# Kernel tuning notes

Hardware: AMD Instinct MI355X
Metric: run time of the kernel (lower is better)

The kernel has to match this reference:

```python
import jax, jax.numpy as jnp
import numpy as np

B, S, D = 2, 1024, 1024
H, KV, HD = 16, 4, 64
E, F = 8, 3584
EPS = 1e-5
TOP_K = 2


def setup_inputs() -> dict:
    key = jax.random.key(0)
    ks = jax.random.split(key, 12)
    sc = 0.02
    inv_freq = 1.0 / (10000.0 ** (np.arange(0, HD, 2, dtype=np.float32) / HD))
    freqs = np.outer(np.arange(S, dtype=np.float32), inv_freq)
    emb = np.concatenate([freqs, freqs], axis=-1)  # [S, HD]
    return {
        'x': jax.random.normal(ks[0], (B, S, D), jnp.float32),
        'ln1_w': jnp.ones((D,), jnp.float32),
        'ln2_w': jnp.ones((D,), jnp.float32),
        'wq': jax.random.normal(ks[1], (H * HD, D), jnp.float32) * sc,
        'wk': jax.random.normal(ks[2], (KV * HD, D), jnp.float32) * sc,
        'wv': jax.random.normal(ks[3], (KV * HD, D), jnp.float32) * sc,
        'wo': jax.random.normal(ks[4], (D, H * HD), jnp.float32) * sc,
        'gate_w': jax.random.normal(ks[5], (E, D), jnp.float32) * sc,
        'w1': jax.random.normal(ks[6], (E, F, D), jnp.float32) * sc,
        'w2': jax.random.normal(ks[7], (E, D, F), jnp.float32) * sc,
        'w3': jax.random.normal(ks[8], (E, F, D), jnp.float32) * sc,
        'cos': jnp.asarray(np.cos(emb)),
        'sin': jnp.asarray(np.sin(emb)),
    }


def _rms_norm(x, w):
    var = jnp.mean(jnp.square(x), axis=-1, keepdims=True)
    return x * jax.lax.rsqrt(var + EPS) * w


def _rotate_half(x):
    x1, x2 = jnp.split(x, 2, axis=-1)
    return jnp.concatenate([-x2, x1], axis=-1)


def _attn(h, wq, wk, wv, wo, cos, sin):
    # h: [B,S,D]
    q = (h @ wq.T).reshape(B, S, H, HD).transpose(0, 2, 1, 3)      # [B,H,S,HD]
    k = (h @ wk.T).reshape(B, S, KV, HD).transpose(0, 2, 1, 3)     # [B,KV,S,HD]
    v = (h @ wv.T).reshape(B, S, KV, HD).transpose(0, 2, 1, 3)
    c = cos[None, None, :S, :]
    s = sin[None, None, :S, :]
    q = q * c + _rotate_half(q) * s
    k = k * c + _rotate_half(k) * s
    k = jnp.repeat(k, H // KV, axis=1)  # GQA expand -> [B,H,S,HD]
    v = jnp.repeat(v, H // KV, axis=1)
    scores = jnp.einsum('bhqd,bhkd->bhqk', q, k) / jnp.sqrt(jnp.float32(HD))
    causal = jnp.tril(jnp.ones((S, S), bool))
    scores = jnp.where(causal[None, None], scores, jnp.float32(-1e30))
    probs = jax.nn.softmax(scores, axis=-1)
    out = jnp.einsum('bhqk,bhkd->bhqd', probs, v)
    out = out.transpose(0, 2, 1, 3).reshape(B, S, H * HD)
    return out @ wo.T


def _moe(h, gate_w, w1, w2, w3):
    T = B * S
    hs = h.reshape(T, D)
    probs = jax.nn.softmax(hs @ gate_w.T, axis=-1)       # [T,E]
    _, sel = jax.lax.top_k(probs, TOP_K)                  # [T,2]
    rw = jnp.take_along_axis(probs, sel, axis=-1)
    rw = rw / jnp.sum(rw, axis=-1, keepdims=True)
    cw = jnp.zeros((T, E), hs.dtype).at[jnp.arange(T)[:, None], sel].add(rw)  # [T,E] combine weights
    h1 = jnp.einsum('td,efd->tef', hs, w1)               # [T,E,F]
    h3 = jnp.einsum('td,efd->tef', hs, w3)
    inter = jax.nn.silu(h1) * h3
    out = jnp.einsum('tef,edf,te->td', inter, w2, cw)
    return out.reshape(B, S, D)


def reference(x, ln1_w, ln2_w, wq, wk, wv, wo, gate_w, w1, w2, w3, cos, sin):
    h = x + _attn(_rms_norm(x, ln1_w), wq, wk, wv, wo, cos, sin)
    h = h + _moe(_rms_norm(h, ln2_w), gate_w, w1, w2, w3)
    return h
```

## Files before the change

kernel.cpp:

```cpp
#include <hip/hip_runtime.h>

typedef unsigned short u16;
using short8 = __attribute__((ext_vector_type(8))) short;
using f32x4  = __attribute__((ext_vector_type(4))) float;

#define TQ   2048
#define DM   1024
#define SLEN 1024
#define FDIM 3584
#define NEXP 8

static __device__ __forceinline__ u16 f2bf(float f) {
  union { float f; unsigned u; } a; a.f = f;
  unsigned r = a.u + 0x7fffu + ((a.u >> 16) & 1u);
  return (u16)(r >> 16);
}
static __device__ __forceinline__ float bf2f(u16 u) {
  union { unsigned u; float f; } a; a.u = ((unsigned)u) << 16;
  return a.f;
}
static __device__ __forceinline__ unsigned cvtpk(float lo, float hi) {
  unsigned r;
  asm volatile("v_cvt_pk_bf16_f32 %0, %1, %2" : "=v"(r) : "v"(lo), "v"(hi));
  return r;
}

static __device__ __forceinline__ void gload16(const void* g, void* l) {
  __builtin_amdgcn_global_load_lds((const __attribute__((address_space(1))) void*)g,
                                   (__attribute__((address_space(3))) void*)l, 16, 0, 0);
}

static __device__ __forceinline__ int swz64(int bid) {
  return (bid & ~63) | ((bid & 7) << 3) | ((bid >> 3) & 7);
}

static __device__ __forceinline__ void cvtwr8(float4 a, float4 b, u16* dst) {
  uint4 u;
  u.x = cvtpk(a.x, a.y); u.y = cvtpk(a.z, a.w);
  u.z = cvtpk(b.x, b.y); u.w = cvtpk(b.z, b.w);
  *(uint4*)dst = u;
}

__global__ __launch_bounds__(256) void rmsnorm_kernel(
    const float* __restrict__ x, const float* __restrict__ w,
    u16* __restrict__ oh, u16* __restrict__ ol, float* __restrict__ of) {
  int t = blockIdx.x, tid = threadIdx.x;
  const float4* xr = (const float4*)(x + (size_t)t * DM);
  float4 v = xr[tid];
  float ss = v.x * v.x + v.y * v.y + v.z * v.z + v.w * v.w;
#pragma unroll
  for (int m = 1; m < 64; m <<= 1) ss += __shfl_xor(ss, m);
  __shared__ float red[4];
  if ((tid & 63) == 0) red[tid >> 6] = ss;
  __syncthreads();
  float tot = red[0] + red[1] + red[2] + red[3];
  float sc = rsqrtf(tot * (1.0f / DM) + 1e-5f);
  float4 wv = ((const float4*)w)[tid];
  float o0 = v.x * sc * wv.x, o1 = v.y * sc * wv.y, o2 = v.z * sc * wv.z, o3 = v.w * sc * wv.w;
  ushort4 hh;
  hh.x = f2bf(o0); hh.y = f2bf(o1); hh.z = f2bf(o2); hh.w = f2bf(o3);
  *(ushort4*)(oh + (size_t)t * DM + tid * 4) = hh;
  if (ol) {
    ushort4 ll;
    ll.x = f2bf(o0 - bf2f(hh.x)); ll.y = f2bf(o1 - bf2f(hh.y));
    ll.z = f2bf(o2 - bf2f(hh.z)); ll.w = f2bf(o3 - bf2f(hh.w));
    *(ushort4*)(ol + (size_t)t * DM + tid * 4) = ll;
  }
  if (of) {
    float4 o4; o4.x = o0; o4.y = o1; o4.z = o2; o4.w = o3;
    ((float4*)(of + (size_t)t * DM))[tid] = o4;
  }
}

__global__ __launch_bounds__(256) void wconv_split_kernel(
    const float* __restrict__ wq, const float* __restrict__ wk,
    const float* __restrict__ wv, const float* __restrict__ wo,
    u16* __restrict__ qkvh, u16* __restrict__ qkvl,
    u16* __restrict__ woh, u16* __restrict__ wol) {
  for (int i = blockIdx.x * 256 + threadIdx.x; i < 655360; i += 640 * 256) {
    int el = i * 4;
    const float* src; u16 *dh, *dl;
    if (el < 1572864) {
      int r = el >> 10, c = el & 1023;
      if (r < 1024) src = wq + el;
      else if (r < 1280) src = wk + (r - 1024) * 1024 + c;
      else src = wv + (r - 1280) * 1024 + c;
      dh = qkvh + el; dl = qkvl + el;
    } else {
      int e2 = el - 1572864;
      src = wo + e2; dh = woh + e2; dl = wol + e2;
    }
    float4 v = *(const float4*)src;
    ushort4 h, l;
    h.x = f2bf(v.x); h.y = f2bf(v.y); h.z = f2bf(v.z); h.w = f2bf(v.w);
    l.x = f2bf(v.x - bf2f(h.x)); l.y = f2bf(v.y - bf2f(h.y));
    l.z = f2bf(v.z - bf2f(h.z)); l.w = f2bf(v.w - bf2f(h.w));
    *(ushort4*)dh = h; *(ushort4*)dl = l;
  }
}

template <bool RESID>
__global__ __launch_bounds__(256) void gemm_split2_kernel(
    const u16* __restrict__ Ah, const u16* __restrict__ Al,
    const u16* __restrict__ Wh, const u16* __restrict__ Wl,
    float* __restrict__ C, const float* __restrict__ resid, int N) {
  __shared__ u16 sAh[2][128][32], sAl[2][128][32], sWh[2][64][32], sWl[2][64][32];
  int lid = swz64(blockIdx.x);
  int bm = lid & 15, bn = lid >> 4;
  int tid = threadIdx.x, lane = tid & 63, w = tid >> 6;
  int wm = w >> 1, wn = w & 1;
  int qi = lane & 15, g = lane >> 4;
  int lr = lane >> 2, lc = (lane & 3) * 8;
  const u16* pa0 = Ah + (size_t)(bm * 128 + w * 16 + lr) * DM + lc;
  const u16* pa1 = pa0 + 64 * DM;
  const u16* pl0 = Al + (size_t)(bm * 128 + w * 16 + lr) * DM + lc;
  const u16* pl1 = pl0 + 64 * DM;
  const u16* pw  = Wh + (size_t)(bn * 64 + w * 16 + lr) * DM + lc;
  const u16* pwl = Wl + (size_t)(bn * 64 + w * 16 + lr) * DM + lc;
  f32x4 acc[4][2] = {};
#define STG2(buf, kk) do { \
    gload16(pa0 + (kk), &sAh[buf][w * 16][0]); \
    gload16(pa1 + (kk), &sAh[buf][64 + w * 16][0]); \
    gload16(pl0 + (kk), &sAl[buf][w * 16][0]); \
    gload16(pl1 + (kk), &sAl[buf][64 + w * 16][0]); \
    gload16(pw  + (kk), &sWh[buf][w * 16][0]); \
    gload16(pwl + (kk), &sWl[buf][w * 16][0]); } while (0)
  STG2(0, 0);
  asm volatile("s_waitcnt vmcnt(0)" ::: "memory");
  __syncthreads();
  for (int ks = 0; ks < 32; ks++) {
    int cur = ks & 1;
    if (ks < 31) STG2(cur ^ 1, (ks + 1) * 32);
    short8 afh[4], afl[4], bfh[2], bfl[2];
#pragma unroll
    for (int i = 0; i < 4; i++) {
      afh[i] = *(short8*)&sAh[cur][wm * 64 + i * 16 + qi][g * 8];
      afl[i] = *(short8*)&sAl[cur][wm * 64 + i * 16 + qi][g * 8];
    }
#pragma unroll
    for (int i = 0; i < 2; i++) {
      bfh[i] = *(short8*)&sWh[cur][wn * 32 + i * 16 + qi][g * 8];
      bfl[i] = *(short8*)&sWl[cur][wn * 32 + i * 16 + qi][g * 8];
    }
#pragma unroll
    for (int mi = 0; mi < 4; mi++)
#pragma unroll
      for (int ni = 0; ni < 2; ni++) {
        f32x4 a = acc[mi][ni];
        a = __builtin_amdgcn_mfma_f32_16x16x32_bf16(afh[mi], bfh[ni], a, 0, 0, 0);
        a = __builtin_amdgcn_mfma_f32_16x16x32_bf16(afl[mi], bfh[ni], a, 0, 0, 0);
        a = __builtin_amdgcn_mfma_f32_16x16x32_bf16(afh[mi], bfl[ni], a, 0, 0, 0);
        acc[mi][ni] = a;
      }
    asm volatile("s_waitcnt vmcnt(0)" ::: "memory");
    __syncthreads();
  }
#undef STG2
#pragma unroll
  for (int mi = 0; mi < 4; mi++)
#pragma unroll
    for (int ni = 0; ni < 2; ni++) {
      int col = bn * 64 + wn * 32 + ni * 16 + qi;
#pragma unroll
      for (int r = 0; r < 4; r++) {
        int row = bm * 128 + wm * 64 + mi * 16 + g * 4 + r;
        float val = acc[mi][ni][r];
        if (RESID) val += resid[(size_t)row * N + col];
        C[(size_t)row * N + col] = val;
      }
    }
}

__global__ __launch_bounds__(256) void rope_split_kernel(
    const float* __restrict__ qkvf,
    const float* __restrict__ cosT, const float* __restrict__ sinT,
    u16* __restrict__ qh, u16* __restrict__ ql, u16* __restrict__ kh, u16* __restrict__ kl,
    u16* __restrict__ vh, u16* __restrict__ vl) {
  int t = blockIdx.x, tid = threadIdx.x;
  int s = t & (SLEN - 1);
  const float* rowp = qkvf + (size_t)t * 1536;
#pragma unroll
  for (int it = 0; it < 2; it++) {
    int i = it * 256 + tid;
    int hh = i >> 5, d = i & 31;
    float c = cosT[s * 64 + d], sn = sinT[s * 64 + d];
    size_t dst = (size_t)t * DM + hh * 64 + d;
    float x1 = rowp[hh * 64 + d], x2 = rowp[hh * 64 + d + 32];
    float o1 = x1 * c - x2 * sn;
    float o2 = x2 * c + x1 * sn;
    u16 h1 = f2bf(o1), h2 = f2bf(o2);
    qh[dst] = h1; qh[dst + 32] = h2;
    ql[dst] = f2bf(o1 - bf2f(h1)); ql[dst + 32] = f2bf(o2 - bf2f(h2));
  }
  if (tid < 128) {
    int hh = tid >> 5, d = tid & 31;
    float c = cosT[s * 64 + d], sn = sinT[s * 64 + d];
    size_t dst = (size_t)t * 256 + hh * 64 + d;
    float x1 = rowp[1024 + hh * 64 + d], x2 = rowp[1024 + hh * 64 + d + 32];
    float o1 = x1 * c - x2 * sn;
    float o2 = x2 * c + x1 * sn;
    u16 h1 = f2bf(o1), h2 = f2bf(o2);
    kh[dst] = h1; kh[dst + 32] = h2;
    kl[dst] = f2bf(o1 - bf2f(h1)); kl[dst + 32] = f2bf(o2 - bf2f(h2));
  }
  {
    size_t dst = (size_t)t * 256 + tid;
    float v = rowp[1280 + tid];
    u16 h = f2bf(v);
    vh[dst] = h; vl[dst] = f2bf(v - bf2f(h));
  }
}

__global__ __launch_bounds__(256) void attn_kernel(
    const u16* __restrict__ qh, const u16* __restrict__ ql,
    const u16* __restrict__ kh, const u16* __restrict__ kl,
    const u16* __restrict__ vh, const u16* __restrict__ vl,
    u16* __restrict__ oh, u16* __restrict__ ol) {
  __shared__ u16 sKh[64][72], sKl[64][72];
  __shared__ u16 sVh[64][72], sVl[64][72];
  __shared__ u16 sPh[4][16][72], sPl[4][16][72];
  int qt = blockIdx.x & 15;
  int bh = blockIdx.x >> 4;
  int b = bh >> 4, h = bh & 15, kvh = h >> 2;
  int tid = threadIdx.x, lane = tid & 63, w = tid >> 6;
  int qi = lane & 15, g = lane >> 4;
  int qrow = qt * 64 + w * 16 + qi;
  size_t qbase = ((size_t)(b * SLEN + qrow)) * DM + h * 64;
  short8 qfh[2], qfl[2];
#pragma unroll
  for (int ds = 0; ds < 2; ds++) {
    qfh[ds] = *(const short8*)(qh + qbase + ds * 32 + g * 8);
    qfl[ds] = *(const short8*)(ql + qbase + ds * 32 + g * 8);
  }
  f32x4 oacc[4] = {};
  float mrun = -1e30f, lrun = 0.f;
  int ktiles = qt + 1;
  for (int kt = 0; kt < ktiles; kt++) {
    __syncthreads();
    {
      int r = tid >> 3, cs = (tid & 7) * 8;
#pragma unroll
      for (int rr = 0; rr < 64; rr += 32) {
        int key = kt * 64 + rr + r;
        size_t src = ((size_t)(b * SLEN + key)) * 256 + kvh * 64 + cs;
        *(short8*)&sKh[rr + r][cs] = *(const short8*)(kh + src);
        *(short8*)&sKl[rr + r][cs] = *(const short8*)(kl + src);
        short8 vv = *(const short8*)(vh + src);
        short8 vv2 = *(const short8*)(vl + src);
#pragma unroll
        for (int j = 0; j < 8; j++) {
          sVh[cs + j][rr + r] = (u16)vv[j];
          sVl[cs + j][rr + r] = (u16)vv2[j];
        }
      }
    }
    __syncthreads();
    f32x4 sa[4];
#pragma unroll
    for (int kf = 0; kf < 4; kf++) {
      f32x4 a = {};
#pragma unroll
      for (int ds = 0; ds < 2; ds++) {
        short8 kfh = *(short8*)&sKh[kf * 16 + qi][ds * 32 + g * 8];
        short8 kfl = *(short8*)&sKl[kf * 16 + qi][ds * 32 + g * 8];
        a = __builtin_amdgcn_mfma_f32_16x16x32_bf16(kfh, qfh[ds], a, 0, 0, 0);
        a = __builtin_amdgcn_mfma_f32_16x16x32_bf16(kfl, qfh[ds], a, 0, 0, 0);
        a = __builtin_amdgcn_mfma_f32_16x16x32_bf16(kfh, qfl[ds], a, 0, 0, 0);
      }
      sa[kf] = a;
    }
    int qg = qt * 64 + w * 16 + qi;
    float sv[4][4];
    float tmax = -1e30f;
#pragma unroll
    for (int kf = 0; kf < 4; kf++)
#pragma unroll
      for (int r = 0; r < 4; r++) {
        int key = kt * 64 + kf * 16 + g * 4 + r;
        float s = sa[kf][r] * 0.125f;
        s = (key <= qg) ? s : -1e30f;
        sv[kf][r] = s;
        tmax = fmaxf(tmax, s);
      }
    tmax = fmaxf(tmax, __shfl_xor(tmax, 16));
    tmax = fmaxf(tmax, __shfl_xor(tmax, 32));
    float mn = fmaxf(mrun, tmax);
    float alpha = expf(mrun - mn);
    float psum = 0.f;
#pragma unroll
    for (int kf = 0; kf < 4; kf++) {
      float p0 = expf(sv[kf][0] - mn), p1 = expf(sv[kf][1] - mn);
      float p2 = expf(sv[kf][2] - mn), p3 = expf(sv[kf][3] - mn);
      psum += p0 + p1 + p2 + p3;
      ushort4 ph, pl;
      ph.x = f2bf(p0); ph.y = f2bf(p1); ph.z = f2bf(p2); ph.w = f2bf(p3);
      pl.x = f2bf(p0 - bf2f(ph.x)); pl.y = f2bf(p1 - bf2f(ph.y));
      pl.z = f2bf(p2 - bf2f(ph.z)); pl.w = f2bf(p3 - bf2f(ph.w));
      *(ushort4*)&sPh[w][qi][kf * 16 + g * 4] = ph;
      *(ushort4*)&sPl[w][qi][kf * 16 + g * 4] = pl;
    }
    psum += __shfl_xor(psum, 16);
    psum += __shfl_xor(psum, 32);
    lrun = lrun * alpha + psum;
    mrun = mn;
#pragma unroll
    for (int df = 0; df < 4; df++) {
      oacc[df][0] *= alpha; oacc[df][1] *= alpha;
      oacc[df][2] *= alpha; oacc[df][3] *= alpha;
    }
#pragma unroll
    for (int ks = 0; ks < 2; ks++) {
      short8 pfh = *(short8*)&sPh[w][qi][ks * 32 + g * 8];
      short8 pfl = *(short8*)&sPl[w][qi][ks * 32 + g * 8];
#pragma unroll
      for (int df = 0; df < 4; df++) {
        short8 vfh = *(short8*)&sVh[df * 16 + qi][ks * 32 + g * 8];
        short8 vfl = *(short8*)&sVl[df * 16 + qi][ks * 32 + g * 8];
        f32x4 a = oacc[df];
        a = __builtin_amdgcn_mfma_f32_16x16x32_bf16(vfh, pfh, a, 0, 0, 0);
        a = __builtin_amdgcn_mfma_f32_16x16x32_bf16(vfl, pfh, a, 0, 0, 0);
        a = __builtin_amdgcn_mfma_f32_16x16x32_bf16(vfh, pfl, a, 0, 0, 0);
        oacc[df] = a;
      }
    }
  }
  float inv = 1.0f / lrun;
  size_t obase = ((size_t)(b * SLEN + qt * 64 + w * 16 + qi)) * DM + h * 64;
#pragma unroll
  for (int df = 0; df < 4; df++) {
    float o0 = oacc[df][0] * inv, o1 = oacc[df][1] * inv;
    float o2 = oacc[df][2] * inv, o3 = oacc[df][3] * inv;
    ushort4 hh, ll;
    hh.x = f2bf(o0); hh.y = f2bf(o1); hh.z = f2bf(o2); hh.w = f2bf(o3);
    ll.x = f2bf(o0 - bf2f(hh.x)); ll.y = f2bf(o1 - bf2f(hh.y));
    ll.z = f2bf(o2 - bf2f(hh.z)); ll.w = f2bf(o3 - bf2f(hh.w));
    *(ushort4*)(oh + obase + df * 16 + g * 4) = hh;
    *(ushort4*)(ol + obase + df * 16 + g * 4) = ll;
  }
}

__global__ void zero8_kernel(int* p) { if (threadIdx.x < 8) p[threadIdx.x] = 0; }

__global__ __launch_bounds__(64) void gate_kernel(
    const float* __restrict__ hf, const float* __restrict__ gw,
    int* cnt, int* tok_e, int* tok_pos, float* tok_w) {
  int t = blockIdx.x, lane = threadIdx.x;
  float acc[8] = {0, 0, 0, 0, 0, 0, 0, 0};
  for (int i = lane; i < DM; i += 64) {
    float h = hf[(size_t)t * DM + i];
#pragma unroll
    for (int e = 0; e < 8; e++) acc[e] += h * gw[e * DM + i];
  }
#pragma unroll
  for (int e = 0; e < 8; e++)
#pragma unroll
    for (int m = 1; m < 64; m <<= 1) acc[e] += __shfl_xor(acc[e], m);
  if (lane == 0) {
    int i0 = 0;
#pragma unroll
    for (int e = 1; e < 8; e++) if (acc[e] > acc[i0]) i0 = e;
    int i1 = -1;
#pragma unroll
    for (int e = 0; e < 8; e++) if (e != i0 && (i1 < 0 || acc[e] > acc[i1])) i1 = e;
    float w0 = 1.0f;
    float w1 = expf(acc[i1] - acc[i0]);
    float rs = 1.0f / (w0 + w1);
    int p0 = atomicAdd(&cnt[i0], 1);
    int p1 = atomicAdd(&cnt[i1], 1);
    tok_e[t * 2] = i0; tok_e[t * 2 + 1] = i1;
    tok_pos[t * 2] = p0; tok_pos[t * 2 + 1] = p1;
    tok_w[t * 2] = w0 * rs; tok_w[t * 2 + 1] = w1 * rs;
  }
}

__global__ void schedule_kernel(const int* cnt, int* offs, int* mt,
                                int* row_e, int* row_bm) {
  if (threadIdx.x == 0) {
    int s = 0, m = 0;
    for (int e = 0; e < 8; e++) {
      offs[e] = s;
      int nb = (cnt[e] + 127) >> 7;
      for (int i = 0; i < nb; i++) { row_e[m] = e; row_bm[m] = i; m++; }
      s += cnt[e];
    }
    *mt = m;
  }
}

__global__ __launch_bounds__(256) void gather_kernel(
    const u16* __restrict__ hn2b, const int* __restrict__ tok_e,
    const int* __restrict__ tok_pos, const float* __restrict__ tok_w,
    const int* __restrict__ offs, u16* __restrict__ Xg,
    int* __restrict__ pair_tok, int* __restrict__ pair_slot, float* __restrict__ pair_w) {
  int t = blockIdx.x;
#pragma unroll
  for (int slot = 0; slot < 2; slot++) {
    int e = tok_e[t * 2 + slot];
    int p = offs[e] + tok_pos[t * 2 + slot];
    ((ushort4*)(Xg + (size_t)p * DM))[threadIdx.x] =
        ((const ushort4*)(hn2b + (size_t)t * DM))[threadIdx.x];
    if (threadIdx.x == 0) {
      pair_tok[p] = t; pair_slot[p] = slot; pair_w[p] = tok_w[t * 2 + slot];
    }
  }
}

__global__ __launch_bounds__(256) void moe_gemm13_kernel(
    const u16* __restrict__ Xg, const float* __restrict__ w1,
    const float* __restrict__ w3, const int* __restrict__ cnt,
    const int* __restrict__ offs, const int* __restrict__ mt,
    const int* __restrict__ row_e, const int* __restrict__ row_bm,
    u16* __restrict__ inter) {
  __shared__ u16 sA[3][128][32];
  __shared__ u16 sW1[3][64][32], sW3[3][64][32];
  int lid = swz64(blockIdx.x);
  int MT = *mt;
  if (lid >= MT * 56) return;
  int mrow = lid % MT, bn = lid / MT;
  int e = row_e[mrow], bm = row_bm[mrow];
  int count = cnt[e], off = offs[e];
  const u16* A = Xg + (size_t)off * DM;
  const float* W1 = w1 + (size_t)e * FDIM * DM;
  const float* W3 = w3 + (size_t)e * FDIM * DM;
  int tid = threadIdx.x, lane = tid & 63, w = tid >> 6;
  int wm = w >> 1, wn = w & 1;
  int qi = lane & 15, g = lane >> 4;
  int lrA = lane >> 2, lcA = (lane & 3) * 8;
  int ga0 = bm * 128 + w * 32 + lrA;      if (ga0 >= count) ga0 = count - 1;
  int ga1 = bm * 128 + w * 32 + 16 + lrA; if (ga1 >= count) ga1 = count - 1;
  const u16* pa0 = A + (size_t)ga0 * DM + lcA;
  const u16* pa1 = A + (size_t)ga1 * DM + lcA;
  int r16 = lane >> 2;
  int rW = w * 16 + r16;
  int cW = (lane & 3) * 8;
  const float* q1 = W1 + (size_t)(bn * 64 + rW) * DM + cW;
  const float* q3 = W3 + (size_t)(bn * 64 + rW) * DM + cW;
  int uW = ((lane & 3) ^ (r16 & 3)) * 8;
  f32x4 acc1[4][2] = {}, acc3[4][2] = {};
  float4 p1a = *(const float4*)q1, p1b = *(const float4*)(q1 + 4);
  float4 p3a = *(const float4*)q3, p3b = *(const float4*)(q3 + 4);
  float4 v1a = *(const float4*)(q1 + 32), v1b = *(const float4*)(q1 + 36);
  float4 v3a = *(const float4*)(q3 + 32), v3b = *(const float4*)(q3 + 36);
  __builtin_amdgcn_sched_barrier(0);
  gload16(pa0, &sA[0][w * 32][0]);
  gload16(pa1, &sA[0][w * 32 + 16][0]);
  gload16(pa0 + 32, &sA[1][w * 32][0]);
  gload16(pa1 + 32, &sA[1][w * 32 + 16][0]);
  asm volatile("s_waitcnt vmcnt(8)" ::: "memory");
  cvtwr8(p1a, p1b, &sW1[0][rW][uW]);
  cvtwr8(p3a, p3b, &sW3[0][rW][uW]);
  for (int ks = 0; ks < 32; ks++) {
    int cur = ks % 3;
    if (ks == 0)       asm volatile("s_waitcnt vmcnt(2) lgkmcnt(0)" ::: "memory");
    else if (ks == 31) asm volatile("s_waitcnt vmcnt(0) lgkmcnt(0)" ::: "memory");
    else               asm volatile("s_waitcnt vmcnt(6) lgkmcnt(0)" ::: "memory");
    __builtin_amdgcn_s_barrier();
    short8 af[4], b1[2], b3[2];
#pragma unroll
    for (int i = 0; i < 4; i++)
      af[i] = *(short8*)&sA[cur][wm * 64 + i * 16 + qi][g * 8];
#pragma unroll
    for (int ni = 0; ni < 2; ni++) {
      int rt = wn * 32 + ni * 16 + qi;
      int ui = (g ^ (rt & 3)) * 8;
      b1[ni] = *(short8*)&sW1[cur][rt][ui];
      b3[ni] = *(short8*)&sW3[cur][rt][ui];
    }
#pragma unroll
    for (int mi = 0; mi < 4; mi++)
#pragma unroll
      for (int ni = 0; ni < 2; ni++) {
        acc1[mi][ni] = __builtin_amdgcn_mfma_f32_16x16x32_bf16(af[mi], b1[ni], acc1[mi][ni], 0, 0, 0);
        acc3[mi][ni] = __builtin_amdgcn_mfma_f32_16x16x32_bf16(af[mi], b3[ni], acc3[mi][ni], 0, 0, 0);
      }
    if (ks < 31) {
      int nb = (ks + 1) % 3;
      cvtwr8(v1a, v1b, &sW1[nb][rW][uW]);
      cvtwr8(v3a, v3b, &sW3[nb][rW][uW]);
      if (ks < 30) {
        int k2 = (ks + 2) * 32;
        v1a = *(const float4*)(q1 + k2); v1b = *(const float4*)(q1 + k2 + 4);
        v3a = *(const float4*)(q3 + k2); v3b = *(const float4*)(q3 + k2 + 4);
        __builtin_amdgcn_sched_barrier(0);
        int ab = (ks + 2) % 3;
        gload16(pa0 + k2, &sA[ab][w * 32][0]);
        gload16(pa1 + k2, &sA[ab][w * 32 + 16][0]);
      }
    }
  }
#pragma unroll
  for (int mi = 0; mi < 4; mi++)
#pragma unroll
    for (int r = 0; r < 4; r++) {
      int row = bm * 128 + wm * 64 + mi * 16 + g * 4 + r;
      if (row < count) {
        size_t obase = (size_t)(off + row) * FDIM + bn * 64 + wn * 32;
#pragma unroll
        for (int ni = 0; ni < 2; ni++) {
          float c1 = acc1[mi][ni][r], c3 = acc3[mi][ni][r];
          float sv = c1 / (1.0f + expf(-c1)) * c3;
          inter[obase + ni * 16 + qi] = f2bf(sv);
        }
      }
    }
}

__global__ __launch_bounds__(256) void moe_gemm2_kernel(
    const u16* __restrict__ inter, const float* __restrict__ w2,
    const int* __restrict__ cnt, const int* __restrict__ offs,
    const int* __restrict__ mt, const int* __restrict__ row_e,
    const int* __restrict__ row_bm,
    const int* __restrict__ pair_tok, const int* __restrict__ pair_slot,
    const float* __restrict__ pair_w, float* __restrict__ pout) {
  __shared__ u16 sA[3][128][32];
  __shared__ u16 sW[3][128][32];
  int lid = swz64(blockIdx.x);
  int MT = *mt;
  if (lid >= MT * 8) return;
  int mrow = lid % MT, bn = lid / MT;
  int e = row_e[mrow], bm = row_bm[mrow];
  int count = cnt[e], off = offs[e];
  const u16* A = inter + (size_t)off * FDIM;
  const float* W = w2 + (size_t)e * DM * FDIM;
  int tid = threadIdx.x, lane = tid & 63, w = tid >> 6;
  int wm = w >> 1, wn = w & 1;
  int qi = lane & 15, g = lane >> 4;
  int lrA = lane >> 2, lcA = (lane & 3) * 8;
  int ga0 = bm * 128 + w * 32 + lrA;      if (ga0 >= count) ga0 = count - 1;
  int ga1 = bm * 128 + w * 32 + 16 + lrA; if (ga1 >= count) ga1 = count - 1;
  const u16* pa0 = A + (size_t)ga0 * FDIM + lcA;
  const u16* pa1 = A + (size_t)ga1 * FDIM + lcA;
  int r32 = lane >> 1;
  int rW = w * 32 + r32;
  int cW = (lane & 1) * 16;
  const float* qw = W + (size_t)(bn * 128 + rW) * FDIM + cW;
  int ug = (lane & 1) * 2;
  int u0 = (ug ^ (r32 & 3)) * 8;
  int u1 = ((ug | 1) ^ (r32 & 3)) * 8;
  f32x4 acc[4][4] = {};
  float4 pa_ = *(const float4*)qw,        pb_ = *(const float4*)(qw + 4);
  float4 pc_ = *(const float4*)(qw + 8),  pd_ = *(const float4*)(qw + 12);
  float4 va = *(const float4*)(qw + 32),  vb = *(const float4*)(qw + 36);
  float4 vc = *(const float4*)(qw + 40),  vd = *(const float4*)(qw + 44);
  __builtin_amdgcn_sched_barrier(0);
  gload16(pa0, &sA[0][w * 32][0]);
  gload16(pa1, &sA[0][w * 32 + 16][0]);
  gload16(pa0 + 32, &sA[1][w * 32][0]);
  gload16(pa1 + 32, &sA[1][w * 32 + 16][0]);
  asm volatile("s_waitcnt vmcnt(8)" ::: "memory");
  cvtwr8(pa_, pb_, &sW[0][rW][u0]);
  cvtwr8(pc_, pd_, &sW[0][rW][u1]);
  const int NK = FDIM / 32;
  for (int ks = 0; ks < NK; ks++) {
    int cur = ks % 3;
    if (ks == 0)           asm volatile("s_waitcnt vmcnt(2) lgkmcnt(0)" ::: "memory");
    else if (ks == NK - 1) asm volatile("s_waitcnt vmcnt(0) lgkmcnt(0)" ::: "memory");
    else                   asm volatile("s_waitcnt vmcnt(6) lgkmcnt(0)" ::: "memory");
    __builtin_amdgcn_s_barrier();
    short8 af[4], bfr[4];
#pragma unroll
    for (int i = 0; i < 4; i++)
      af[i] = *(short8*)&sA[cur][wm * 64 + i * 16 + qi][g * 8];
#pragma unroll
    for (int ni = 0; ni < 4; ni++) {
      int rt = wn * 64 + ni * 16 + qi;
      bfr[ni] = *(short8*)&sW[cur][rt][(g ^ (rt & 3)) * 8];
    }
#pragma unroll
    for (int mi = 0; mi < 4; mi++)
#pragma unroll
      for (int ni = 0; ni < 4; ni++)
        acc[mi][ni] = __builtin_amdgcn_mfma_f32_16x16x32_bf16(af[mi], bfr[ni], acc[mi][ni], 0, 0, 0);
    if (ks < NK - 1) {
      int nb = (ks + 1) % 3;
      cvtwr8(va, vb, &sW[nb][rW][u0]);
      cvtwr8(vc, vd, &sW[nb][rW][u1]);
      if (ks < NK - 2) {
        int k2 = (ks + 2) * 32;
        va = *(const float4*)(qw + k2);      vb = *(const float4*)(qw + k2 + 4);
        vc = *(const float4*)(qw + k2 + 8);  vd = *(const float4*)(qw + k2 + 12);
        __builtin_amdgcn_sched_barrier(0);
        int ab = (ks + 2) % 3;
        gload16(pa0 + k2, &sA[ab][w * 32][0]);
        gload16(pa1 + k2, &sA[ab][w * 32 + 16][0]);
      }
    }
  }
#pragma unroll
  for (int mi = 0; mi < 4; mi++)
#pragma unroll
    for (int r = 0; r < 4; r++) {
      int row = bm * 128 + wm * 64 + mi * 16 + g * 4 + r;
      if (row < count) {
        int p = off + row;
        int t = pair_tok[p];
        float wgt = pair_w[p];
        size_t obase = ((size_t)pair_slot[p] * TQ + t) * DM + bn * 128 + wn * 64;
#pragma unroll
        for (int ni = 0; ni < 4; ni++)
          pout[obase + ni * 16 + qi] = acc[mi][ni][r] * wgt;
      }
    }
}

__global__ __launch_bounds__(256) void combine_kernel(
    const float* __restrict__ h, const float* __restrict__ pout, float* __restrict__ out) {
  size_t i = (size_t)blockIdx.x * 256 + threadIdx.x;
  float4 a = ((const float4*)h)[i];
  float4 b0 = ((const float4*)pout)[i];
  float4 b1 = ((const float4*)pout)[i + (size_t)TQ * DM / 4];
  float4 r;
  r.x = a.x + b0.x + b1.x; r.y = a.y + b0.y + b1.y;
  r.z = a.z + b0.z + b1.z; r.w = a.w + b0.w + b1.w;
  ((float4*)out)[i] = r;
}

extern "C" void kernel_launch(void* const* d_in, const int* in_sizes, int n_in,
                              void* d_out, int out_size, void* d_ws, size_t ws_size,
                              hipStream_t stream) {
  (void)in_sizes; (void)n_in; (void)out_size; (void)ws_size;
  const float* x    = (const float*)d_in[0];
  const float* ln1  = (const float*)d_in[1];
  const float* ln2  = (const float*)d_in[2];
  const float* wq   = (const float*)d_in[3];
  const float* wk   = (const float*)d_in[4];
  const float* wv   = (const float*)d_in[5];
  const float* wo   = (const float*)d_in[6];
  const float* gw   = (const float*)d_in[7];
  const float* w1   = (const float*)d_in[8];
  const float* w2   = (const float*)d_in[9];
  const float* w3   = (const float*)d_in[10];
  const float* cosT = (const float*)d_in[11];
  const float* sinT = (const float*)d_in[12];

  char* mb = (char*)d_ws;
  const size_t MB = 1024 * 1024;
  u16*   qhb  = (u16*)(mb + 0 * MB);
  u16*   qlb  = (u16*)(mb + 4 * MB);
  u16*   khb  = (u16*)(mb + 8 * MB);
  u16*   klb  = (u16*)(mb + 9 * MB);
  u16*   vhb  = (u16*)(mb + 10 * MB);
  u16*   vlb  = (u16*)(mb + 11 * MB);
  u16*   hn2b = (u16*)(mb + 0 * MB);
  float* hn2f = (float*)(mb + 4 * MB);
  u16*   ahb  = (u16*)(mb + 12 * MB);
  u16*   alb  = (u16*)(mb + 16 * MB);
  u16*   Xg   = (u16*)(mb + 12 * MB);
  u16*   hn1h = (u16*)(mb + 20 * MB);
  u16*   hn1l = (u16*)(mb + 24 * MB);
  u16*   inter= (u16*)(mb + 20 * MB);
  float* qkvf = (float*)(mb + 28 * MB);
  float* h_res= (float*)(mb + 48 * MB);
  u16*   woh  = (u16*)(mb + 56 * MB);
  u16*   wol  = (u16*)(mb + 58 * MB);
  float* pout = (float*)(mb + 56 * MB);
  u16*   wqkvh= (u16*)(mb + 60 * MB);
  u16*   wqkvl= (u16*)(mb + 63 * MB);
  int*   cnt  = (int*)(mb + 72 * MB);
  int*   offs = cnt + 8;
  int*   mtp  = cnt + 16;
  int*   row_e  = cnt + 17;
  int*   row_bm = cnt + 57;
  int*   tok_e  = cnt + 128;
  int*   tok_pos = tok_e + 4096;
  float* tok_w   = (float*)(tok_pos + 4096);
  int*   pair_tok  = (int*)(tok_w + 4096);
  int*   pair_slot = pair_tok + 4096;
  float* pair_w    = (float*)(pair_slot + 4096);

  wconv_split_kernel<<<640, 256, 0, stream>>>(wq, wk, wv, wo, wqkvh, wqkvl, woh, wol);
  rmsnorm_kernel<<<TQ, 256, 0, stream>>>(x, ln1, hn1h, hn1l, nullptr);
  gemm_split2_kernel<false><<<384, 256, 0, stream>>>(hn1h, hn1l, wqkvh, wqkvl, qkvf, nullptr, 1536);
  rope_split_kernel<<<TQ, 256, 0, stream>>>(qkvf, cosT, sinT, qhb, qlb, khb, klb, vhb, vlb);
  attn_kernel<<<512, 256, 0, stream>>>(qhb, qlb, khb, klb, vhb, vlb, ahb, alb);
  gemm_split2_kernel<true><<<256, 256, 0, stream>>>(ahb, alb, woh, wol, h_res, x, 1024);
  rmsnorm_kernel<<<TQ, 256, 0, stream>>>(h_res, ln2, hn2b, nullptr, hn2f);
  zero8_kernel<<<1, 64, 0, stream>>>(cnt);
  gate_kernel<<<TQ, 64, 0, stream>>>(hn2f, gw, cnt, tok_e, tok_pos, tok_w);
  schedule_kernel<<<1, 64, 0, stream>>>(cnt, offs, mtp, row_e, row_bm);
  gather_kernel<<<TQ, 256, 0, stream>>>(hn2b, tok_e, tok_pos, tok_w, offs, Xg,
                                        pair_tok, pair_slot, pair_w);
  moe_gemm13_kernel<<<2240, 256, 0, stream>>>(Xg, w1, w3, cnt, offs, mtp,
                                              row_e, row_bm, inter);
  moe_gemm2_kernel<<<320, 256, 0, stream>>>(inter, w2, cnt, offs, mtp,
                                            row_e, row_bm,
                                            pair_tok, pair_slot, pair_w, pout);
  combine_kernel<<<TQ, 256, 0, stream>>>(h_res, pout, (float*)d_out);
}
```

Measured before the change: 510.2 us.

## Store MoE GEMM LDS tiles in MFMA fragment order and raise MFMA priority

Both MoE GEMM kernels now write the A and weight tiles into LDS already arranged in MFMA fragment order. Each lane can then read its short8 operand with one contiguous lane*8 access, with no XOR swizzle or row indexing. The global load mapping changes to match, and the weight rows are split into two strided halves in gemm2. The modulo-3 buffer index becomes a rotating counter, and s_setprio wraps the MFMA block to favour math issue. The aim is to cut LDS bank conflicts and address arithmetic, though the new global access pattern may coalesce less well.

```diff
diff --git a/kernel.cpp b/kernel.cpp
--- a/kernel.cpp
+++ b/kernel.cpp
@@ -411,8 +411,8 @@
     const int* __restrict__ offs, const int* __restrict__ mt,
     const int* __restrict__ row_e, const int* __restrict__ row_bm,
     u16* __restrict__ inter) {
-  __shared__ u16 sA[3][128][32];
-  __shared__ u16 sW1[3][64][32], sW3[3][64][32];
+  __shared__ u16 sA[3][4096];
+  __shared__ u16 sW1[3][2048], sW3[3][2048];
   int lid = swz64(blockIdx.x);
   int MT = *mt;
   if (lid >= MT * 56) return;
@@ -425,47 +425,50 @@
   int tid = threadIdx.x, lane = tid & 63, w = tid >> 6;
   int wm = w >> 1, wn = w & 1;
   int qi = lane & 15, g = lane >> 4;
-  int lrA = lane >> 2, lcA = (lane & 3) * 8;
-  int ga0 = bm * 128 + w * 32 + lrA;      if (ga0 >= count) ga0 = count - 1;
-  int ga1 = bm * 128 + w * 32 + 16 + lrA; if (ga1 >= count) ga1 = count - 1;
-  const u16* pa0 = A + (size_t)ga0 * DM + lcA;
-  const u16* pa1 = A + (size_t)ga1 * DM + lcA;
-  int r16 = lane >> 2;
-  int rW = w * 16 + r16;
-  int cW = (lane & 3) * 8;
-  const float* q1 = W1 + (size_t)(bn * 64 + rW) * DM + cW;
-  const float* q3 = W3 + (size_t)(bn * 64 + rW) * DM + cW;
-  int uW = ((lane & 3) ^ (r16 & 3)) * 8;
+  int f0 = 2 * w, f1 = 2 * w + 1;
+  int rA0 = (f0 >> 2) * 64 + (f0 & 3) * 16 + qi;
+  int rA1 = (f1 >> 2) * 64 + (f1 & 3) * 16 + qi;
+  int cA = g * 8;
+  int g0 = bm * 128 + rA0; if (g0 >= count) g0 = count - 1;
+  int g1 = bm * 128 + rA1; if (g1 >= count) g1 = count - 1;
+  const u16* pa0 = A + (size_t)g0 * DM + cA;
+  const u16* pa1 = A + (size_t)g1 * DM + cA;
+  int rW = (tid >> 7) * 32 + ((tid >> 6) & 1) * 16 + (tid & 15);
+  int cWf = ((tid >> 4) & 3) * 8;
+  const float* q1 = W1 + (size_t)(bn * 64 + rW) * DM + cWf;
+  const float* q3 = W3 + (size_t)(bn * 64 + rW) * DM + cWf;
   f32x4 acc1[4][2] = {}, acc3[4][2] = {};
   float4 p1a = *(const float4*)q1, p1b = *(const float4*)(q1 + 4);
   float4 p3a = *(const float4*)q3, p3b = *(const float4*)(q3 + 4);
   float4 v1a = *(const float4*)(q1 + 32), v1b = *(const float4*)(q1 + 36);
   float4 v3a = *(const float4*)(q3 + 32), v3b = *(const float4*)(q3 + 36);
   __builtin_amdgcn_sched_barrier(0);
-  gload16(pa0, &sA[0][w * 32][0]);
-  gload16(pa1, &sA[0][w * 32 + 16][0]);
-  gload16(pa0 + 32, &sA[1][w * 32][0]);
-  gload16(pa1 + 32, &sA[1][w * 32 + 16][0]);
+  gload16(pa0, &sA[0][f0 * 512]);
+  gload16(pa1, &sA[0][f1 * 512]);
+  gload16(pa0 + 32, &sA[1][f0 * 512]);
+  gload16(pa1 + 32, &sA[1][f1 * 512]);
   asm volatile("s_waitcnt vmcnt(8)" ::: "memory");
-  cvtwr8(p1a, p1b, &sW1[0][rW][uW]);
-  cvtwr8(p3a, p3b, &sW3[0][rW][uW]);
+  cvtwr8(p1a, p1b, &sW1[0][tid * 8]);
+  cvtwr8(p3a, p3b, &sW3[0][tid * 8]);
+  int cur = 0;
   for (int ks = 0; ks < 32; ks++) {
-    int cur = ks % 3;
     if (ks == 0)       asm volatile("s_waitcnt vmcnt(2) lgkmcnt(0)" ::: "memory");
     else if (ks == 31) asm volatile("s_waitcnt vmcnt(0) lgkmcnt(0)" ::: "memory");
     else               asm volatile("s_waitcnt vmcnt(6) lgkmcnt(0)" ::: "memory");
     __builtin_amdgcn_s_barrier();
+    const u16* sa = &sA[cur][0];
+    const u16* s1 = &sW1[cur][0];
+    const u16* s3 = &sW3[cur][0];
     short8 af[4], b1[2], b3[2];
 #pragma unroll
     for (int i = 0; i < 4; i++)
-      af[i] = *(short8*)&sA[cur][wm * 64 + i * 16 + qi][g * 8];
+      af[i] = *(const short8*)(sa + (wm * 4 + i) * 512 + lane * 8);
 #pragma unroll
     for (int ni = 0; ni < 2; ni++) {
-      int rt = wn * 32 + ni * 16 + qi;
-      int ui = (g ^ (rt & 3)) * 8;
-      b1[ni] = *(short8*)&sW1[cur][rt][ui];
-      b3[ni] = *(short8*)&sW3[cur][rt][ui];
-    }
+      b1[ni] = *(const short8*)(s1 + (wn * 2 + ni) * 512 + lane * 8);
+      b3[ni] = *(const short8*)(s3 + (wn * 2 + ni) * 512 + lane * 8);
+    }
+    __builtin_amdgcn_s_setprio(1);
 #pragma unroll
     for (int mi = 0; mi < 4; mi++)
 #pragma unroll
@@ -473,20 +476,22 @@
         acc1[mi][ni] = __builtin_amdgcn_mfma_f32_16x16x32_bf16(af[mi], b1[ni], acc1[mi][ni], 0, 0, 0);
         acc3[mi][ni] = __builtin_amdgcn_mfma_f32_16x16x32_bf16(af[mi], b3[ni], acc3[mi][ni], 0, 0, 0);
       }
+    __builtin_amdgcn_s_setprio(0);
     if (ks < 31) {
-      int nb = (ks + 1) % 3;
-      cvtwr8(v1a, v1b, &sW1[nb][rW][uW]);
-      cvtwr8(v3a, v3b, &sW3[nb][rW][uW]);
+      int nb = (cur == 2) ? 0 : cur + 1;
+      cvtwr8(v1a, v1b, &sW1[nb][tid * 8]);
+      cvtwr8(v3a, v3b, &sW3[nb][tid * 8]);
       if (ks < 30) {
         int k2 = (ks + 2) * 32;
         v1a = *(const float4*)(q1 + k2); v1b = *(const float4*)(q1 + k2 + 4);
         v3a = *(const float4*)(q3 + k2); v3b = *(const float4*)(q3 + k2 + 4);
         __builtin_amdgcn_sched_barrier(0);
-        int ab = (ks + 2) % 3;
-        gload16(pa0 + k2, &sA[ab][w * 32][0]);
-        gload16(pa1 + k2, &sA[ab][w * 32 + 16][0]);
-      }
-    }
+        int pb = (nb == 2) ? 0 : nb + 1;
+        gload16(pa0 + k2, &sA[pb][f0 * 512]);
+        gload16(pa1 + k2, &sA[pb][f1 * 512]);
+      }
+    }
+    cur = (cur == 2) ? 0 : cur + 1;
   }
 #pragma unroll
   for (int mi = 0; mi < 4; mi++)
@@ -512,8 +517,8 @@
     const int* __restrict__ row_bm,
     const int* __restrict__ pair_tok, const int* __restrict__ pair_slot,
     const float* __restrict__ pair_w, float* __restrict__ pout) {
-  __shared__ u16 sA[3][128][32];
-  __shared__ u16 sW[3][128][32];
+  __shared__ u16 sA[3][4096];
+  __shared__ u16 sW[3][4096];
   int lid = swz64(blockIdx.x);
   int MT = *mt;
   if (lid >= MT * 8) return;
@@ -525,66 +530,69 @@
   int tid = threadIdx.x, lane = tid & 63, w = tid >> 6;
   int wm = w >> 1, wn = w & 1;
   int qi = lane & 15, g = lane >> 4;
-  int lrA = lane >> 2, lcA = (lane & 3) * 8;
-  int ga0 = bm * 128 + w * 32 + lrA;      if (ga0 >= count) ga0 = count - 1;
-  int ga1 = bm * 128 + w * 32 + 16 + lrA; if (ga1 >= count) ga1 = count - 1;
-  const u16* pa0 = A + (size_t)ga0 * FDIM + lcA;
-  const u16* pa1 = A + (size_t)ga1 * FDIM + lcA;
-  int r32 = lane >> 1;
-  int rW = w * 32 + r32;
-  int cW = (lane & 1) * 16;
-  const float* qw = W + (size_t)(bn * 128 + rW) * FDIM + cW;
-  int ug = (lane & 1) * 2;
-  int u0 = (ug ^ (r32 & 3)) * 8;
-  int u1 = ((ug | 1) ^ (r32 & 3)) * 8;
+  int f0 = 2 * w, f1 = 2 * w + 1;
+  int rA0 = (f0 >> 2) * 64 + (f0 & 3) * 16 + qi;
+  int rA1 = (f1 >> 2) * 64 + (f1 & 3) * 16 + qi;
+  int cA = g * 8;
+  int g0 = bm * 128 + rA0; if (g0 >= count) g0 = count - 1;
+  int g1 = bm * 128 + rA1; if (g1 >= count) g1 = count - 1;
+  const u16* pa0 = A + (size_t)g0 * FDIM + cA;
+  const u16* pa1 = A + (size_t)g1 * FDIM + cA;
+  int rW0 = ((tid >> 6) & 3) * 16 + (tid & 15);
+  int cWf = ((tid >> 4) & 3) * 8;
+  const float* qw0 = W + (size_t)(bn * 128 + rW0) * FDIM + cWf;
+  const float* qw1 = qw0 + (size_t)64 * FDIM;
   f32x4 acc[4][4] = {};
-  float4 pa_ = *(const float4*)qw,        pb_ = *(const float4*)(qw + 4);
-  float4 pc_ = *(const float4*)(qw + 8),  pd_ = *(const float4*)(qw + 12);
-  float4 va = *(const float4*)(qw + 32),  vb = *(const float4*)(qw + 36);
-  float4 vc = *(const float4*)(qw + 40),  vd = *(const float4*)(qw + 44);
+  float4 pa_ = *(const float4*)qw0, pb_ = *(const float4*)(qw0 + 4);
+  float4 pc_ = *(const float4*)qw1, pd_ = *(const float4*)(qw1 + 4);
+  float4 va = *(const float4*)(qw0 + 32), vb = *(const float4*)(qw0 + 36);
+  float4 vc = *(const float4*)(qw1 + 32), vd = *(const float4*)(qw1 + 36);
   __builtin_amdgcn_sched_barrier(0);
-  gload16(pa0, &sA[0][w * 32][0]);
-  gload16(pa1, &sA[0][w * 32 + 16][0]);
-  gload16(pa0 + 32, &sA[1][w * 32][0]);
-  gload16(pa1 + 32, &sA[1][w * 32 + 16][0]);
+  gload16(pa0, &sA[0][f0 * 512]);
+  gload16(pa1, &sA[0][f1 * 512]);
+  gload16(pa0 + 32, &sA[1][f0 * 512]);
+  gload16(pa1 + 32, &sA[1][f1 * 512]);
   asm volatile("s_waitcnt vmcnt(8)" ::: "memory");
-  cvtwr8(pa_, pb_, &sW[0][rW][u0]);
-  cvtwr8(pc_, pd_, &sW[0][rW][u1]);
+  cvtwr8(pa_, pb_, &sW[0][tid * 8]);
+  cvtwr8(pc_, pd_, &sW[0][2048 + tid * 8]);
   const int NK = FDIM / 32;
+  int cur = 0;
   for (int ks = 0; ks < NK; ks++) {
-    int cur = ks % 3;
     if (ks == 0)           asm volatile("s_waitcnt vmcnt(2) lgkmcnt(0)" ::: "memory");
     else if (ks == NK - 1) asm volatile("s_waitcnt vmcnt(0) lgkmcnt(0)" ::: "memory");
     else                   asm volatile("s_waitcnt vmcnt(6) lgkmcnt(0)" ::: "memory");
     __builtin_amdgcn_s_barrier();
+    const u16* sa = &sA[cur][0];
+    const u16* sw = &sW[cur][0];
     short8 af[4], bfr[4];
 #pragma unroll
     for (int i = 0; i < 4; i++)
-      af[i] = *(short8*)&sA[cur][wm * 64 + i * 16 + qi][g * 8];
-#pragma unroll
-    for (int ni = 0; ni < 4; ni++) {
-      int rt = wn * 64 + ni * 16 + qi;
-      bfr[ni] = *(short8*)&sW[cur][rt][(g ^ (rt & 3)) * 8];
-    }
+      af[i] = *(const short8*)(sa + (wm * 4 + i) * 512 + lane * 8);
+#pragma unroll
+    for (int ni = 0; ni < 4; ni++)
+      bfr[ni] = *(const short8*)(sw + (wn * 4 + ni) * 512 + lane * 8);
+    __builtin_amdgcn_s_setprio(1);
 #pragma unroll
     for (int mi = 0; mi < 4; mi++)
 #pragma unroll
       for (int ni = 0; ni < 4; ni++)
         acc[mi][ni] = __builtin_amdgcn_mfma_f32_16x16x32_bf16(af[mi], bfr[ni], acc[mi][ni], 0, 0, 0);
+    __builtin_amdgcn_s_setprio(0);
     if (ks < NK - 1) {
-      int nb = (ks + 1) % 3;
-      cvtwr8(va, vb, &sW[nb][rW][u0]);
-      cvtwr8(vc, vd, &sW[nb][rW][u1]);
+      int nb = (cur == 2) ? 0 : cur + 1;
+      cvtwr8(va, vb, &sW[nb][tid * 8]);
+      cvtwr8(vc, vd, &sW[nb][2048 + tid * 8]);
       if (ks < NK - 2) {
         int k2 = (ks + 2) * 32;
-        va = *(const float4*)(qw + k2);      vb = *(const float4*)(qw + k2 + 4);
-        vc = *(const float4*)(qw + k2 + 8);  vd = *(const float4*)(qw + k2 + 12);
+        va = *(const float4*)(qw0 + k2); vb = *(const float4*)(qw0 + k2 + 4);
+        vc = *(const float4*)(qw1 + k2); vd = *(const float4*)(qw1 + k2 + 4);
         __builtin_amdgcn_sched_barrier(0);
-        int ab = (ks + 2) % 3;
-        gload16(pa0 + k2, &sA[ab][w * 32][0]);
-        gload16(pa1 + k2, &sA[ab][w * 32 + 16][0]);
-      }
-    }
+        int pb = (nb == 2) ? 0 : nb + 1;
+        gload16(pa0 + k2, &sA[pb][f0 * 512]);
+        gload16(pa1 + k2, &sA[pb][f1 * 512]);
+      }
+    }
+    cur = (cur == 2) ? 0 : cur + 1;
   }
 #pragma unroll
   for (int mi = 0; mi < 4; mi++)
```

After: 598.1 us. +17.2%, slower.
